# Kernel optimization log

Hardware: AMD Instinct MI355X
Metric: run time of the kernel (lower is better)

The kernel has to match this reference:

```python
import jax, jax.numpy as jnp
import numpy as np

T, N, M = 16, 10000, 2048          # timesteps, total nodes, masked nodes per step
F_IN, F1, F2, H = 256, 256, 256, 256  # feats_per_node, layer_1, layer_2, lstm_feats


def setup_inputs() -> dict:
    key = jax.random.key(0)
    ks = jax.random.split(key, 9)
    A = jax.random.normal(ks[0], (T, M, M), jnp.float32) / np.float32(np.sqrt(M))
    node_feats = jax.random.normal(ks[1], (N, F_IN), jnp.float32)
    # unique sorted indices per timestep (scatter target must be duplicate-free)
    mask = jax.vmap(lambda k: jnp.sort(jax.random.permutation(k, N)[:M]))(
        jax.random.split(ks[2], T)).astype(jnp.int32)
    u = lambda k, sh, fan: jax.random.uniform(k, sh, jnp.float32, -1.0, 1.0) * (2.0 / np.sqrt(fan))
    w0 = u(ks[3], (F_IN, F1), F_IN)
    w1 = u(ks[4], (F1, F2), F1)
    s = 1.0 / np.sqrt(H)
    W_ih = jax.random.uniform(ks[5], (4 * H, F2), jnp.float32, -s, s)
    W_hh = jax.random.uniform(ks[6], (4 * H, H), jnp.float32, -s, s)
    b_ih = jax.random.uniform(ks[7], (4 * H,), jnp.float32, -s, s)
    b_hh = jax.random.uniform(ks[8], (4 * H,), jnp.float32, -s, s)
    return {"A": A, "node_feats": node_feats, "mask": mask, "w0": w0, "w1": w1,
            "W_ih": W_ih, "W_hh": W_hh, "b_ih": b_ih, "b_hh": b_hh}


def reference(A, node_feats, mask, w0, w1, W_ih, W_hh, b_ih, b_hh):
    def gcn_step(Ah, idx):
        # layer 0: x = X @ W0 ; x[idx] = act(Ahat @ x[idx])
        x = node_feats @ w0                               # [N, F1]
        x = x.at[idx].set(jax.nn.relu(Ah @ x[idx]))
        # layer 1
        x = x @ w1                                        # [N, F2]
        x = x.at[idx].set(jax.nn.relu(Ah @ x[idx]))
        return x

    seq = jax.vmap(gcn_step)(A, mask)                     # [T, N, F2]

    def lstm_step(carry, xt):
        h, c = carry
        z = xt @ W_ih.T + h @ W_hh.T + (b_ih + b_hh)      # [N, 4H]
        i, f, g, o = jnp.split(z, 4, axis=-1)             # torch gate order i,f,g,o
        c = jax.nn.sigmoid(f) * c + jax.nn.sigmoid(i) * jnp.tanh(g)
        h = jax.nn.sigmoid(o) * jnp.tanh(c)
        return (h, c), None

    h0 = jnp.zeros((N, H), seq.dtype)
    (h, _), _ = jax.lax.scan(lstm_step, (h0, h0), seq)
    return h                                              # out[-1] of single-layer LSTM
```

## Files before the change

kernel.cpp:

```cpp
#include <hip/hip_runtime.h>
#include <cstdint>
#include <cstddef>

#pragma clang diagnostic ignored "-Waddress-space-conversion"

constexpr int T  = 16;
constexpr int N  = 10000;
constexpr int M  = 2048;
constexpr int F  = 256;
constexpr int H  = 256;
constexpr int G4 = 1024;
constexpr int NP = 10112;

typedef _Float16 f16;
using half8  = __attribute__((ext_vector_type(8))) f16;
using half4  = __attribute__((ext_vector_type(4))) f16;
using f32x4  = __attribute__((ext_vector_type(4))) float;

typedef __attribute__((address_space(1))) const void gas_t;
typedef __attribute__((address_space(3))) void las_t;

__device__ __forceinline__ void gl_lds16(const f16* g, f16* l) {
    __builtin_amdgcn_global_load_lds((gas_t*)g, (las_t*)l, 16, 0, 0);
}

__device__ __forceinline__ float fast_tanh(float x) {
    const float ax = fabsf(x);
    const float e  = __expf(-2.f * ax);
    const float t  = (1.f - e) / (1.f + e);
    return copysignf(t, x);
}

template<bool AF32, bool RELU, int OMODE>
__global__ __launch_bounds__(256, 2)
void gemm16(const void* __restrict__ Ag, long long sA,
            const f16*  __restrict__ Bg, long long sB,
            void*       __restrict__ Cg, long long sC,
            int Kk, int Nn, int Mvalid, int ldct)
{
    __shared__ f16 Als[2][128 * 32];
    __shared__ f16 Bls[2][128 * 32];

    const int tid  = threadIdx.x;
    const int lane = tid & 63;
    const int w    = tid >> 6;
    const int wm   = w >> 1, wn = w & 1;
    const int m0   = blockIdx.y * 128, n0 = blockIdx.x * 128;
    const int z    = blockIdx.z;

    const f16* Bt = Bg + (size_t)z * sB;
    const int srow = lane >> 2;
    const int scol = (lane & 3) * 8;

    f32x4 acc[4][4] = {};

    auto stage = [&](int buf, int kt) {
        const int k0 = kt * 32;
        #pragma unroll
        for (int c = 0; c < 2; ++c) {
            const int brow = w * 32 + c * 16;
            gl_lds16(Bt + (size_t)(n0 + brow + srow) * Kk + k0 + scol,
                     &Bls[buf][brow * 32]);
        }
        if constexpr (AF32) {
            const float* Af = (const float*)Ag + (size_t)z * sA;
            #pragma unroll
            for (int p = 0; p < 4; ++p) {
                const int flat = p * 1024 + tid * 4;
                const int r = flat >> 5, cc = flat & 31;
                float4 v = *(const float4*)&Af[(size_t)(m0 + r) * Kk + k0 + cc];
                half4 hv = { (f16)v.x, (f16)v.y, (f16)v.z, (f16)v.w };
                *(half4*)&Als[buf][r * 32 + cc] = hv;
            }
        } else {
            const f16* Af = (const f16*)Ag + (size_t)z * sA;
            #pragma unroll
            for (int c = 0; c < 2; ++c) {
                const int arow = w * 32 + c * 16;
                gl_lds16(Af + (size_t)(m0 + arow + srow) * Kk + k0 + scol,
                         &Als[buf][arow * 32]);
            }
        }
    };

    const int nk = Kk >> 5;
    stage(0, 0);
    int cur = 0;
    const int fr = lane & 15, fg = lane >> 4;

    for (int kt = 0; kt < nk; ++kt) {
        __syncthreads();
        if (kt + 1 < nk) stage(cur ^ 1, kt + 1);

        half8 a[4], b[4];
        #pragma unroll
        for (int i = 0; i < 4; ++i)
            a[i] = *(const half8*)&Als[cur][(wm * 64 + i * 16 + fr) * 32 + fg * 8];
        #pragma unroll
        for (int j = 0; j < 4; ++j)
            b[j] = *(const half8*)&Bls[cur][(wn * 64 + j * 16 + fr) * 32 + fg * 8];
        #pragma unroll
        for (int i = 0; i < 4; ++i)
            #pragma unroll
            for (int j = 0; j < 4; ++j)
                acc[i][j] = __builtin_amdgcn_mfma_f32_16x16x32_f16(a[i], b[j], acc[i][j], 0, 0, 0);
        cur ^= 1;
    }

    #pragma unroll
    for (int i = 0; i < 4; ++i) {
        const int gmb = m0 + wm * 64 + i * 16 + fg * 4;
        #pragma unroll
        for (int j = 0; j < 4; ++j) {
            const int gn = n0 + wn * 64 + j * 16 + fr;
            f32x4 v = acc[i][j];
            if (RELU) {
                v[0] = fmaxf(v[0], 0.f); v[1] = fmaxf(v[1], 0.f);
                v[2] = fmaxf(v[2], 0.f); v[3] = fmaxf(v[3], 0.f);
            }
            if constexpr (OMODE == 1) {
                f16* Ch = (f16*)Cg + (size_t)z * sC;
                #pragma unroll
                for (int r = 0; r < 4; ++r)
                    if (gmb + r < Mvalid) Ch[(size_t)(gmb + r) * Nn + gn] = (f16)v[r];
            } else {
                f16* Ct = (f16*)Cg + (size_t)z * sC;
                half4 hv = { (f16)v[0], (f16)v[1], (f16)v[2], (f16)v[3] };
                if (gmb + 3 < Mvalid) *(half4*)&Ct[(size_t)gn * ldct + gmb] = hv;
            }
        }
    }
}

__global__ __launch_bounds__(256, 2)
void gemm_lstm(const f16* __restrict__ h16, const f16* __restrict__ Whh,
               const f16* __restrict__ U, const f16* __restrict__ V,
               const int* __restrict__ invt, const float* __restrict__ bsum,
               float* __restrict__ Cb, f16* __restrict__ h16_out,
               float* __restrict__ hout)
{
    __shared__ f16 Als[2][128 * 32];
    __shared__ f16 Bls[2][128 * 32];

    const int tid  = threadIdx.x;
    const int lane = tid & 63;
    const int w    = tid >> 6;
    const int wm   = w >> 1, wn = w & 1;
    const int m0   = blockIdx.y * 128, n0 = blockIdx.x * 128;

    const int srow = lane >> 2;
    const int scol = (lane & 3) * 8;

    f32x4 acc[4][4] = {};

    auto stage = [&](int buf, int kt) {
        const int k0 = kt * 32;
        #pragma unroll
        for (int c = 0; c < 2; ++c) {
            const int row = w * 32 + c * 16;
            gl_lds16(Whh + (size_t)(n0 + row + srow) * H + k0 + scol, &Bls[buf][row * 32]);
            gl_lds16(h16 + (size_t)(m0 + row + srow) * H + k0 + scol, &Als[buf][row * 32]);
        }
    };

    stage(0, 0);
    int cur = 0;
    const int fr = lane & 15, fg = lane >> 4;

    for (int kt = 0; kt < H / 32; ++kt) {
        __syncthreads();
        if (kt + 1 < H / 32) stage(cur ^ 1, kt + 1);
        half8 a[4], b[4];
        #pragma unroll
        for (int i = 0; i < 4; ++i)
            a[i] = *(const half8*)&Als[cur][(wm * 64 + i * 16 + fr) * 32 + fg * 8];
        #pragma unroll
        for (int j = 0; j < 4; ++j)
            b[j] = *(const half8*)&Bls[cur][(wn * 64 + j * 16 + fr) * 32 + fg * 8];
        #pragma unroll
        for (int i = 0; i < 4; ++i)
            #pragma unroll
            for (int j = 0; j < 4; ++j)
                acc[i][j] = __builtin_amdgcn_mfma_f32_16x16x32_f16(a[i], b[j], acc[i][j], 0, 0, 0);
        cur ^= 1;
    }

    const int u = ((n0 >> 6) + wn) * 16 + fr;
    const int colbase = n0 + wn * 64 + fr;
    const float b0 = bsum[colbase], b1 = bsum[colbase + 16],
                b2 = bsum[colbase + 32], b3 = bsum[colbase + 48];
    auto sig = [](float x) { return 1.f / (1.f + __expf(-x)); };

    #pragma unroll
    for (int i = 0; i < 4; ++i) {
        const int nodeb = m0 + wm * 64 + i * 16 + fg * 4;
        #pragma unroll
        for (int r = 0; r < 4; ++r) {
            const int node = nodeb + r;
            if (node >= N) continue;
            const int p = invt[node];
            const f16* xb = (p >= 0) ? V + (size_t)p * G4 : U + (size_t)node * G4;
            const float zi = acc[i][0][r] + (float)xb[colbase]      + b0;
            const float zf = acc[i][1][r] + (float)xb[colbase + 16] + b1;
            const float zg = acc[i][2][r] + (float)xb[colbase + 32] + b2;
            const float zo = acc[i][3][r] + (float)xb[colbase + 48] + b3;
            const size_t ci = (size_t)node * H + u;
            const float c = sig(zf) * Cb[ci] + sig(zi) * fast_tanh(zg);
            Cb[ci] = c;
            const float hv = sig(zo) * fast_tanh(c);
            h16_out[ci] = (f16)hv;
            if (hout) hout[ci] = hv;
        }
    }
}

__global__ __launch_bounds__(256)
void gather_T(const f16* __restrict__ Y0h, const int* __restrict__ mask,
              f16* __restrict__ GT)
{
    __shared__ f16 tile[64][F + 8];
    const int t = blockIdx.y, p0 = blockIdx.x * 64;
    const int tid = threadIdx.x;
    const int pr = tid >> 2;
    const int fc = (tid & 3) * 8;

    const int row = mask[t * M + p0 + pr];
    const f16* src = Y0h + (size_t)row * F;
    #pragma unroll
    for (int it = 0; it < 8; ++it) {
        const int f = it * 32 + fc;
        *(half8*)&tile[pr][f] = *(const half8*)&src[f];
    }
    __syncthreads();

    f16* dst = GT + ((size_t)t * F + tid) * M + p0;
    #pragma unroll
    for (int pc = 0; pc < 64; pc += 8) {
        half8 v;
        #pragma unroll
        for (int r = 0; r < 8; ++r) v[r] = tile[pc + r][tid];
        *(half8*)&dst[pc] = v;
    }
}

__global__ void cvt_f16(const float* __restrict__ s, f16* __restrict__ d, long long n)
{
    long long base = ((long long)blockIdx.x * blockDim.x + threadIdx.x) * 4;
    if (base + 3 < n) {
        float4 v = *(const float4*)&s[base];
        half4 hv = { (f16)v.x, (f16)v.y, (f16)v.z, (f16)v.w };
        *(half4*)&d[base] = hv;
    } else {
        for (long long k = base; k < n; ++k) d[k] = (f16)s[k];
    }
}

__global__ void cvtT_f16(const float* __restrict__ s, f16* __restrict__ d, int R, int C)
{
    int i = blockIdx.x * 256 + threadIdx.x;
    if (i >= R * C) return;
    int r = i % R, c = i / R;
    d[(size_t)c * R + r] = (f16)s[(size_t)r * C + c];
}

__global__ void permW(const float* __restrict__ s, f16* __restrict__ d, int K)
{
    const int pcol = blockIdx.x;
    const int c64 = pcol >> 6, within = pcol & 63, gate = within >> 4, r = within & 15;
    const int srow = gate * 256 + c64 * 16 + r;
    const float* sp = s + (size_t)srow * K;
    f16* dp = d + (size_t)pcol * K;
    const int k = threadIdx.x * 4;
    float4 v = *(const float4*)&sp[k];
    half4 hv = { (f16)v.x, (f16)v.y, (f16)v.z, (f16)v.w };
    *(half4*)&dp[k] = hv;
}

__global__ void bias_perm(const float* __restrict__ bi, const float* __restrict__ bh,
                          float* __restrict__ bsum)
{
    const int pcol = blockIdx.x * 256 + threadIdx.x;
    if (pcol >= G4) return;
    const int c64 = pcol >> 6, within = pcol & 63, gate = within >> 4, r = within & 15;
    const int srow = gate * 256 + c64 * 16 + r;
    bsum[pcol] = bi[srow] + bh[srow];
}

__global__ void build_inv(const int* __restrict__ mask, int* __restrict__ inv)
{
    int i = blockIdx.x * blockDim.x + threadIdx.x;
    if (i >= T * M) return;
    int t = i / M;
    inv[(size_t)t * N + mask[i]] = i % M;
}

extern "C" void kernel_launch(void* const* d_in, const int* in_sizes, int n_in,
                              void* d_out, int out_size, void* d_ws, size_t ws_size,
                              hipStream_t stream)
{
    const float* A_all = (const float*)d_in[0];
    const float* nf    = (const float*)d_in[1];
    const int*   mask  = (const int*)  d_in[2];
    const float* w0    = (const float*)d_in[3];
    const float* w1    = (const float*)d_in[4];
    const float* W_ih  = (const float*)d_in[5];
    const float* W_hh  = (const float*)d_in[6];
    const float* b_ih  = (const float*)d_in[7];
    const float* b_hh  = (const float*)d_in[8];
    float* h = (float*)d_out;

    char* wp = (char*)d_ws;
    auto alloc = [&](size_t bytes) { char* p = wp; wp += (bytes + 255) & ~(size_t)255; return p; };
    f16*   nf16  = (f16*)alloc((size_t)NP * F * 2);
    f16*   w0T   = (f16*)alloc((size_t)F * F * 2);
    f16*   w1T   = (f16*)alloc((size_t)F * F * 2);
    f16*   Wih16 = (f16*)alloc((size_t)G4 * F * 2);
    f16*   Whh16 = (f16*)alloc((size_t)G4 * H * 2);
    float* bsum  = (float*)alloc((size_t)G4 * 4);
    f16*   Y0h   = (f16*)alloc((size_t)NP * F * 2);
    f16*   Y1h   = (f16*)alloc((size_t)NP * F * 2);
    f16*   Uh    = (f16*)alloc((size_t)NP * G4 * 2);
    f16*   GT    = (f16*)alloc((size_t)T * F * M * 2);
    f16*   Z1b   = (f16*)alloc((size_t)T * M * F * 2);
    f16*   Z2T   = (f16*)alloc((size_t)T * F * M * 2);
    f16*   Z3b   = (f16*)alloc((size_t)T * M * F * 2);
    f16*   Vb    = (f16*)alloc((size_t)4 * M * G4 * 2);
    float* Cb    = (float*)alloc((size_t)N * H * 4);
    f16*   h16   = (f16*)alloc((size_t)NP * H * 2);
    int*   inv   = (int*)alloc((size_t)T * N * 4);

    const size_t a16_bytes = (size_t)T * M * M * 2;
    const size_t used      = (size_t)(wp - (char*)d_ws);
    const bool   useA16    = (used + a16_bytes) <= ws_size;
    f16* A16 = useA16 ? (f16*)alloc(a16_bytes) : nullptr;

    hipMemsetAsync(Cb,  0,    (size_t)N * H * 4,  stream);
    hipMemsetAsync(h16, 0,    (size_t)NP * H * 2, stream);
    hipMemsetAsync(nf16,0,    (size_t)NP * F * 2, stream);
    hipMemsetAsync(inv, 0xFF, (size_t)T * N * 4,  stream);

    build_inv<<<(T * M + 255) / 256, 256, 0, stream>>>(mask, inv);
    cvt_f16 <<<((long long)N * F / 4 + 255) / 256, 256, 0, stream>>>(nf, nf16, (long long)N * F);
    cvtT_f16<<<(F * F + 255) / 256, 256, 0, stream>>>(w0, w0T, F, F);
    cvtT_f16<<<(F * F + 255) / 256, 256, 0, stream>>>(w1, w1T, F, F);
    permW<<<G4, 64, 0, stream>>>(W_ih, Wih16, F);
    permW<<<G4, 64, 0, stream>>>(W_hh, Whh16, H);
    bias_perm<<<(G4 + 255) / 256, 256, 0, stream>>>(b_ih, b_hh, bsum);

    gemm16<false,false,1><<<dim3(F / 128,  NP / 128, 1), 256, 0, stream>>>(nf16, 0, w0T,   0, Y0h, 0, F, F,  NP, 0);
    gemm16<false,false,1><<<dim3(F / 128,  NP / 128, 1), 256, 0, stream>>>(Y0h,  0, w1T,   0, Y1h, 0, F, F,  NP, 0);
    gemm16<false,false,1><<<dim3(G4 / 128, NP / 128, 1), 256, 0, stream>>>(Y1h,  0, Wih16, 0, Uh,  0, F, G4, NP, 0);

    gather_T<<<dim3(M / 64, T), 256, 0, stream>>>(Y0h, mask, GT);

    const long long sAmm = (long long)M * M;
    const long long sFM  = (long long)F * M;
    const long long sMF  = (long long)M * F;

    if (useA16) {
        cvt_f16<<<(int)(((long long)T * M * M / 4 + 255) / 256), 256, 0, stream>>>(
            A_all, A16, (long long)T * M * M);
        gemm16<false,true, 1><<<dim3(2, 16, T), 256, 0, stream>>>(A16, sAmm, GT,  sFM, Z1b, sMF, M, F, M, 0);
        gemm16<false,false,2><<<dim3(2, 16, T), 256, 0, stream>>>(Z1b, sMF,  w1T, 0,   Z2T, sFM, F, F, M, M);
        gemm16<false,true, 1><<<dim3(2, 16, T), 256, 0, stream>>>(A16, sAmm, Z2T, sFM, Z3b, sMF, M, F, M, 0);
    } else {
        gemm16<true, true, 1><<<dim3(2, 16, T), 256, 0, stream>>>(A_all, sAmm, GT,  sFM, Z1b, sMF, M, F, M, 0);
        gemm16<false,false,2><<<dim3(2, 16, T), 256, 0, stream>>>(Z1b,  sMF,  w1T, 0,   Z2T, sFM, F, F, M, M);
        gemm16<true, true, 1><<<dim3(2, 16, T), 256, 0, stream>>>(A_all, sAmm, Z2T, sFM, Z3b, sMF, M, F, M, 0);
    }

    for (int t = 0; t < T; ++t) {
        if ((t & 3) == 0) {
            gemm16<false,false,1><<<dim3(G4 / 128, M / 128, 4), 256, 0, stream>>>(
                Z3b + (size_t)t * M * F, sMF, Wih16, 0, Vb, (long long)M * G4, F, G4, M, 0);
        }
        gemm_lstm<<<dim3(G4 / 128, NP / 128, 1), 256, 0, stream>>>(
            h16, Whh16, Uh, Vb + (size_t)(t & 3) * M * G4, inv + (size_t)t * N,
            bsum, Cb, h16, (t == T - 1) ? h : nullptr);
    }
}
```

Before: 765.6 us.

## Fold weight chain into Uh, fuse A fp16 conversion into first GEMM, raise LSTM occupancy

Precomputes Wih·w1ᵀ·w0ᵀ as a small 1024x256 matrix so the unmasked gate inputs Uh come from one GEMM on node features, dropping the intermediate Y1h GEMM over all nodes. The standalone fp32-to-fp16 conversion pass over A is removed. Instead the first adjacency GEMM writes the converted fp16 tiles back to workspace from the n0==0 blocks, which the third GEMM then reads. gemm_lstm launch bounds go from 2 to 3 waves per SIMD, which may cause register spills. The weight reassociation changes fp16 rounding order.

```diff
diff --git a/kernel.cpp b/kernel.cpp
--- a/kernel.cpp
+++ b/kernel.cpp
@@ -31,12 +31,13 @@
     return copysignf(t, x);
 }
 
-template<bool AF32, bool RELU, int OMODE>
+template<bool AF32, bool RELU, int OMODE, bool AWB>
 __global__ __launch_bounds__(256, 2)
 void gemm16(const void* __restrict__ Ag, long long sA,
             const f16*  __restrict__ Bg, long long sB,
             void*       __restrict__ Cg, long long sC,
-            int Kk, int Nn, int Mvalid, int ldct)
+            int Kk, int Nn, int Mvalid, int ldct,
+            f16* __restrict__ a16wb)
 {
     __shared__ f16 Als[2][128 * 32];
     __shared__ f16 Bls[2][128 * 32];
@@ -71,6 +72,10 @@
                 float4 v = *(const float4*)&Af[(size_t)(m0 + r) * Kk + k0 + cc];
                 half4 hv = { (f16)v.x, (f16)v.y, (f16)v.z, (f16)v.w };
                 *(half4*)&Als[buf][r * 32 + cc] = hv;
+                if constexpr (AWB) {
+                    if (n0 == 0)
+                        *(half4*)&a16wb[(size_t)z * sA + (size_t)(m0 + r) * Kk + k0 + cc] = hv;
+                }
             }
         } else {
             const f16* Af = (const f16*)Ag + (size_t)z * sA;
@@ -132,7 +137,7 @@
     }
 }
 
-__global__ __launch_bounds__(256, 2)
+__global__ __launch_bounds__(256, 3)
 void gemm_lstm(const f16* __restrict__ h16, const f16* __restrict__ Whh,
                const f16* __restrict__ U, const f16* __restrict__ V,
                const int* __restrict__ invt, const float* __restrict__ bsum,
@@ -314,11 +319,14 @@
     f16*   nf16  = (f16*)alloc((size_t)NP * F * 2);
     f16*   w0T   = (f16*)alloc((size_t)F * F * 2);
     f16*   w1T   = (f16*)alloc((size_t)F * F * 2);
+    f16*   w0f   = (f16*)alloc((size_t)F * F * 2);
+    f16*   w1f   = (f16*)alloc((size_t)F * F * 2);
     f16*   Wih16 = (f16*)alloc((size_t)G4 * F * 2);
     f16*   Whh16 = (f16*)alloc((size_t)G4 * H * 2);
+    f16*   S1    = (f16*)alloc((size_t)G4 * F * 2);
+    f16*   S2    = (f16*)alloc((size_t)G4 * F * 2);
     float* bsum  = (float*)alloc((size_t)G4 * 4);
     f16*   Y0h   = (f16*)alloc((size_t)NP * F * 2);
-    f16*   Y1h   = (f16*)alloc((size_t)NP * F * 2);
     f16*   Uh    = (f16*)alloc((size_t)NP * G4 * 2);
     f16*   GT    = (f16*)alloc((size_t)T * F * M * 2);
     f16*   Z1b   = (f16*)alloc((size_t)T * M * F * 2);
@@ -343,13 +351,17 @@
     cvt_f16 <<<((long long)N * F / 4 + 255) / 256, 256, 0, stream>>>(nf, nf16, (long long)N * F);
     cvtT_f16<<<(F * F + 255) / 256, 256, 0, stream>>>(w0, w0T, F, F);
     cvtT_f16<<<(F * F + 255) / 256, 256, 0, stream>>>(w1, w1T, F, F);
+    cvt_f16 <<<(F * F / 4 + 255) / 256, 256, 0, stream>>>(w0, w0f, (long long)F * F);
+    cvt_f16 <<<(F * F / 4 + 255) / 256, 256, 0, stream>>>(w1, w1f, (long long)F * F);
     permW<<<G4, 64, 0, stream>>>(W_ih, Wih16, F);
     permW<<<G4, 64, 0, stream>>>(W_hh, Whh16, H);
     bias_perm<<<(G4 + 255) / 256, 256, 0, stream>>>(b_ih, b_hh, bsum);
 
-    gemm16<false,false,1><<<dim3(F / 128,  NP / 128, 1), 256, 0, stream>>>(nf16, 0, w0T,   0, Y0h, 0, F, F,  NP, 0);
-    gemm16<false,false,1><<<dim3(F / 128,  NP / 128, 1), 256, 0, stream>>>(Y0h,  0, w1T,   0, Y1h, 0, F, F,  NP, 0);
-    gemm16<false,false,1><<<dim3(G4 / 128, NP / 128, 1), 256, 0, stream>>>(Y1h,  0, Wih16, 0, Uh,  0, F, G4, NP, 0);
+    gemm16<false,false,1,false><<<dim3(2, 8, 1), 256, 0, stream>>>(Wih16, 0, w1f, 0, S1, 0, F, F, G4, 0, nullptr);
+    gemm16<false,false,1,false><<<dim3(2, 8, 1), 256, 0, stream>>>(S1,    0, w0f, 0, S2, 0, F, F, G4, 0, nullptr);
+
+    gemm16<false,false,1,false><<<dim3(F / 128,  NP / 128, 1), 256, 0, stream>>>(nf16, 0, w0T, 0, Y0h, 0, F, F,  NP, 0, nullptr);
+    gemm16<false,false,1,false><<<dim3(G4 / 128, NP / 128, 1), 256, 0, stream>>>(nf16, 0, S2,  0, Uh,  0, F, G4, NP, 0, nullptr);
 
     gather_T<<<dim3(M / 64, T), 256, 0, stream>>>(Y0h, mask, GT);
 
@@ -358,21 +370,19 @@
     const long long sMF  = (long long)M * F;
 
     if (useA16) {
-        cvt_f16<<<(int)(((long long)T * M * M / 4 + 255) / 256), 256, 0, stream>>>(
-            A_all, A16, (long long)T * M * M);
-        gemm16<false,true, 1><<<dim3(2, 16, T), 256, 0, stream>>>(A16, sAmm, GT,  sFM, Z1b, sMF, M, F, M, 0);
-        gemm16<false,false,2><<<dim3(2, 16, T), 256, 0, stream>>>(Z1b, sMF,  w1T, 0,   Z2T, sFM, F, F, M, M);
-        gemm16<false,true, 1><<<dim3(2, 16, T), 256, 0, stream>>>(A16, sAmm, Z2T, sFM, Z3b, sMF, M, F, M, 0);
+        gemm16<true, true, 1,true ><<<dim3(2, 16, T), 256, 0, stream>>>(A_all, sAmm, GT,  sFM, Z1b, sMF, M, F, M, 0, A16);
+        gemm16<false,false,2,false><<<dim3(2, 16, T), 256, 0, stream>>>(Z1b,  sMF,  w1T, 0,   Z2T, sFM, F, F, M, M, nullptr);
+        gemm16<false,true, 1,false><<<dim3(2, 16, T), 256, 0, stream>>>(A16,  sAmm, Z2T, sFM, Z3b, sMF, M, F, M, 0, nullptr);
     } else {
-        gemm16<true, true, 1><<<dim3(2, 16, T), 256, 0, stream>>>(A_all, sAmm, GT,  sFM, Z1b, sMF, M, F, M, 0);
-        gemm16<false,false,2><<<dim3(2, 16, T), 256, 0, stream>>>(Z1b,  sMF,  w1T, 0,   Z2T, sFM, F, F, M, M);
-        gemm16<true, true, 1><<<dim3(2, 16, T), 256, 0, stream>>>(A_all, sAmm, Z2T, sFM, Z3b, sMF, M, F, M, 0);
+        gemm16<true, true, 1,false><<<dim3(2, 16, T), 256, 0, stream>>>(A_all, sAmm, GT,  sFM, Z1b, sMF, M, F, M, 0, nullptr);
+        gemm16<false,false,2,false><<<dim3(2, 16, T), 256, 0, stream>>>(Z1b,  sMF,  w1T, 0,   Z2T, sFM, F, F, M, M, nullptr);
+        gemm16<true, true, 1,false><<<dim3(2, 16, T), 256, 0, stream>>>(A_all, sAmm, Z2T, sFM, Z3b, sMF, M, F, M, 0, nullptr);
     }
 
     for (int t = 0; t < T; ++t) {
         if ((t & 3) == 0) {
-            gemm16<false,false,1><<<dim3(G4 / 128, M / 128, 4), 256, 0, stream>>>(
-                Z3b + (size_t)t * M * F, sMF, Wih16, 0, Vb, (long long)M * G4, F, G4, M, 0);
+            gemm16<false,false,1,false><<<dim3(G4 / 128, M / 128, 4), 256, 0, stream>>>(
+                Z3b + (size_t)t * M * F, sMF, Wih16, 0, Vb, (long long)M * G4, F, G4, M, 0, nullptr);
         }
         gemm_lstm<<<dim3(G4 / 128, NP / 128, 1), 256, 0, stream>>>(
             h16, Whh16, Uh, Vb + (size_t)(t & 3) * M * G4, inv + (size_t)t * N,
```

Result: slower. 883.5 us (+15.4%).

## Fuse LSTM timesteps into one persistent cooperative kernel with grid sync

Applied to the files above, without the earlier changes.

Replaces the 16 per-timestep gemm_lstm launches with one cooperative kernel. It loops over timesteps, keeps the cell state in registers and ping-pongs h between two buffers, with grid.sync between steps. The V projection for all timesteps is computed up front in a single batched GEMM instead of in chunks of four. This removes launch overhead and the global read/write of C, but grid-wide sync costs something each step, and 640 blocks must be co-resident (3 per CU across 256 CUs). If that does not fit, it falls back to the per-step launches.

```diff
diff --git a/kernel.cpp b/kernel.cpp
--- a/kernel.cpp
+++ b/kernel.cpp
@@ -1,16 +1,20 @@
 #include <hip/hip_runtime.h>
+#include <hip/hip_cooperative_groups.h>
 #include <cstdint>
 #include <cstddef>
 
 #pragma clang diagnostic ignored "-Waddress-space-conversion"
 
-constexpr int T  = 16;
-constexpr int N  = 10000;
-constexpr int M  = 2048;
-constexpr int F  = 256;
-constexpr int H  = 256;
-constexpr int G4 = 1024;
-constexpr int NP = 10112;
+namespace cg = cooperative_groups;
+
+constexpr int T   = 16;
+constexpr int N   = 10000;
+constexpr int M   = 2048;
+constexpr int F   = 256;
+constexpr int H   = 256;
+constexpr int G4  = 1024;
+constexpr int NP  = 10112;
+constexpr int NP2 = 10240;
 
 typedef _Float16 f16;
 using half8  = __attribute__((ext_vector_type(8))) f16;
@@ -132,11 +136,102 @@
     }
 }
 
+__global__ __launch_bounds__(256, 3)
+void lstm_chain(const f16* __restrict__ Whh, const f16* __restrict__ U,
+                const f16* __restrict__ Vall, const int* __restrict__ invall,
+                const float* __restrict__ bsum,
+                f16* __restrict__ ha, f16* __restrict__ hb,
+                float* __restrict__ hout)
+{
+    cg::grid_group grid = cg::this_grid();
+    __shared__ f16 Als[2][128 * 32];
+    __shared__ f16 Bls[2][128 * 32];
+
+    const int tid  = threadIdx.x;
+    const int lane = tid & 63;
+    const int w    = tid >> 6;
+    const int wm   = w >> 1, wn = w & 1;
+    const int m0   = blockIdx.x * 128;
+    const int n0   = blockIdx.y * 128;
+    const int srow = lane >> 2, scol = (lane & 3) * 8;
+    const int fr   = lane & 15, fg = lane >> 4;
+
+    const int u = ((n0 >> 6) + wn) * 16 + fr;
+    const int colbase = n0 + wn * 64 + fr;
+    const float b0 = bsum[colbase],      b1 = bsum[colbase + 16],
+                b2 = bsum[colbase + 32], b3 = bsum[colbase + 48];
+    auto sig = [](float x) { return 1.f / (1.f + __expf(-x)); };
+
+    float creg[4][4] = {};
+    const f16* hin = ha;
+    f16*       hnx = hb;
+
+    for (int t = 0; t < T; ++t) {
+        const f16* V    = Vall   + (size_t)t * M * G4;
+        const int* invt = invall + (size_t)t * N;
+
+        f32x4 acc[4][4] = {};
+        auto stageh = [&](int buf, int kt) {
+            const int k0 = kt * 32;
+            #pragma unroll
+            for (int c = 0; c < 2; ++c) {
+                const int row = w * 32 + c * 16;
+                gl_lds16(Whh + (size_t)(n0 + row + srow) * H + k0 + scol, &Bls[buf][row * 32]);
+                gl_lds16(hin + (size_t)(m0 + row + srow) * H + k0 + scol, &Als[buf][row * 32]);
+            }
+        };
+        stageh(0, 0);
+        int cur = 0;
+        #pragma unroll
+        for (int kt = 0; kt < H / 32; ++kt) {
+            __syncthreads();
+            if (kt + 1 < H / 32) stageh(cur ^ 1, kt + 1);
+            half8 a[4], b[4];
+            #pragma unroll
+            for (int i = 0; i < 4; ++i)
+                a[i] = *(const half8*)&Als[cur][(wm * 64 + i * 16 + fr) * 32 + fg * 8];
+            #pragma unroll
+            for (int j = 0; j < 4; ++j)
+                b[j] = *(const half8*)&Bls[cur][(wn * 64 + j * 16 + fr) * 32 + fg * 8];
+            #pragma unroll
+            for (int i = 0; i < 4; ++i)
+                #pragma unroll
+                for (int j = 0; j < 4; ++j)
+                    acc[i][j] = __builtin_amdgcn_mfma_f32_16x16x32_f16(a[i], b[j], acc[i][j], 0, 0, 0);
+            cur ^= 1;
+        }
+
+        #pragma unroll
+        for (int i = 0; i < 4; ++i) {
+            const int nodeb = m0 + wm * 64 + i * 16 + fg * 4;
+            #pragma unroll
+            for (int r = 0; r < 4; ++r) {
+                const int node = nodeb + r;
+                if (node < N) {
+                    const int p = invt[node];
+                    const f16* xb = (p >= 0) ? V + (size_t)p * G4 : U + (size_t)node * G4;
+                    const float zi = acc[i][0][r] + (float)xb[colbase]      + b0;
+                    const float zf = acc[i][1][r] + (float)xb[colbase + 16] + b1;
+                    const float zg = acc[i][2][r] + (float)xb[colbase + 32] + b2;
+                    const float zo = acc[i][3][r] + (float)xb[colbase + 48] + b3;
+                    const float c  = sig(zf) * creg[i][r] + sig(zi) * fast_tanh(zg);
+                    creg[i][r] = c;
+                    const float hv = sig(zo) * fast_tanh(c);
+                    hnx[(size_t)node * H + u] = (f16)hv;
+                    if (t == T - 1) hout[(size_t)node * H + u] = hv;
+                }
+            }
+        }
+        grid.sync();
+        f16* tmp = (f16*)hin; hin = hnx; hnx = tmp;
+    }
+}
+
 __global__ __launch_bounds__(256, 2)
-void gemm_lstm(const f16* __restrict__ h16, const f16* __restrict__ Whh,
+void gemm_lstm(const f16* __restrict__ hin, const f16* __restrict__ Whh,
                const f16* __restrict__ U, const f16* __restrict__ V,
                const int* __restrict__ invt, const float* __restrict__ bsum,
-               float* __restrict__ Cb, f16* __restrict__ h16_out,
+               float* __restrict__ Cb, f16* __restrict__ hout16,
                float* __restrict__ hout)
 {
     __shared__ f16 Als[2][128 * 32];
@@ -147,9 +242,7 @@
     const int w    = tid >> 6;
     const int wm   = w >> 1, wn = w & 1;
     const int m0   = blockIdx.y * 128, n0 = blockIdx.x * 128;
-
-    const int srow = lane >> 2;
-    const int scol = (lane & 3) * 8;
+    const int srow = lane >> 2, scol = (lane & 3) * 8;
 
     f32x4 acc[4][4] = {};
 
@@ -159,7 +252,7 @@
         for (int c = 0; c < 2; ++c) {
             const int row = w * 32 + c * 16;
             gl_lds16(Whh + (size_t)(n0 + row + srow) * H + k0 + scol, &Bls[buf][row * 32]);
-            gl_lds16(h16 + (size_t)(m0 + row + srow) * H + k0 + scol, &Als[buf][row * 32]);
+            gl_lds16(hin + (size_t)(m0 + row + srow) * H + k0 + scol, &Als[buf][row * 32]);
         }
     };
 
@@ -187,7 +280,7 @@
 
     const int u = ((n0 >> 6) + wn) * 16 + fr;
     const int colbase = n0 + wn * 64 + fr;
-    const float b0 = bsum[colbase], b1 = bsum[colbase + 16],
+    const float b0 = bsum[colbase],      b1 = bsum[colbase + 16],
                 b2 = bsum[colbase + 32], b3 = bsum[colbase + 48];
     auto sig = [](float x) { return 1.f / (1.f + __expf(-x)); };
 
@@ -208,7 +301,7 @@
             const float c = sig(zf) * Cb[ci] + sig(zi) * fast_tanh(zg);
             Cb[ci] = c;
             const float hv = sig(zo) * fast_tanh(c);
-            h16_out[ci] = (f16)hv;
+            hout16[ci] = (f16)hv;
             if (hout) hout[ci] = hv;
         }
     }
@@ -324,9 +417,10 @@
     f16*   Z1b   = (f16*)alloc((size_t)T * M * F * 2);
     f16*   Z2T   = (f16*)alloc((size_t)T * F * M * 2);
     f16*   Z3b   = (f16*)alloc((size_t)T * M * F * 2);
-    f16*   Vb    = (f16*)alloc((size_t)4 * M * G4 * 2);
+    f16*   Vb    = (f16*)alloc((size_t)T * M * G4 * 2);
     float* Cb    = (float*)alloc((size_t)N * H * 4);
-    f16*   h16   = (f16*)alloc((size_t)NP * H * 2);
+    f16*   h16a  = (f16*)alloc((size_t)NP2 * H * 2);
+    f16*   h16b  = (f16*)alloc((size_t)NP2 * H * 2);
     int*   inv   = (int*)alloc((size_t)T * N * 4);
 
     const size_t a16_bytes = (size_t)T * M * M * 2;
@@ -334,10 +428,11 @@
     const bool   useA16    = (used + a16_bytes) <= ws_size;
     f16* A16 = useA16 ? (f16*)alloc(a16_bytes) : nullptr;
 
-    hipMemsetAsync(Cb,  0,    (size_t)N * H * 4,  stream);
-    hipMemsetAsync(h16, 0,    (size_t)NP * H * 2, stream);
-    hipMemsetAsync(nf16,0,    (size_t)NP * F * 2, stream);
-    hipMemsetAsync(inv, 0xFF, (size_t)T * N * 4,  stream);
+    hipMemsetAsync(Cb,   0,    (size_t)N * H * 4,    stream);
+    hipMemsetAsync(h16a, 0,    (size_t)NP2 * H * 2,  stream);
+    hipMemsetAsync(h16b, 0,    (size_t)NP2 * H * 2,  stream);
+    hipMemsetAsync(nf16, 0,    (size_t)NP * F * 2,   stream);
+    hipMemsetAsync(inv,  0xFF, (size_t)T * N * 4,    stream);
 
     build_inv<<<(T * M + 255) / 256, 256, 0, stream>>>(mask, inv);
     cvt_f16 <<<((long long)N * F / 4 + 255) / 256, 256, 0, stream>>>(nf, nf16, (long long)N * F);
@@ -369,13 +464,28 @@
         gemm16<true, true, 1><<<dim3(2, 16, T), 256, 0, stream>>>(A_all, sAmm, Z2T, sFM, Z3b, sMF, M, F, M, 0);
     }
 
-    for (int t = 0; t < T; ++t) {
-        if ((t & 3) == 0) {
-            gemm16<false,false,1><<<dim3(G4 / 128, M / 128, 4), 256, 0, stream>>>(
-                Z3b + (size_t)t * M * F, sMF, Wih16, 0, Vb, (long long)M * G4, F, G4, M, 0);
-        }
-        gemm_lstm<<<dim3(G4 / 128, NP / 128, 1), 256, 0, stream>>>(
-            h16, Whh16, Uh, Vb + (size_t)(t & 3) * M * G4, inv + (size_t)t * N,
-            bsum, Cb, h16, (t == T - 1) ? h : nullptr);
-    }
-}
+    gemm16<false,false,1><<<dim3(G4 / 128, M / 128, T), 256, 0, stream>>>(
+        Z3b, sMF, Wih16, 0, Vb, (long long)M * G4, F, G4, M, 0);
+
+    constexpr int NB_CHAIN = (NP2 / 128) * (G4 / 128);
+    int occ = 0;
+    bool coop = (hipOccupancyMaxActiveBlocksPerMultiprocessor(&occ, lstm_chain, 256, 0)
+                 == hipSuccess) && (occ * 256 >= NB_CHAIN);
+    if (coop) {
+        void* args[] = { (void*)&Whh16, (void*)&Uh, (void*)&Vb, (void*)&inv,
+                         (void*)&bsum, (void*)&h16a, (void*)&h16b, (void*)&h };
+        coop = hipLaunchCooperativeKernel((void*)lstm_chain, dim3(NP2 / 128, G4 / 128, 1),
+                                          dim3(256, 1, 1), args, 0, stream) == hipSuccess;
+        if (!coop) (void)hipGetLastError();
+    }
+    if (!coop) {
+        const f16* hin = h16a;
+        f16*       hnx = h16b;
+        for (int t = 0; t < T; ++t) {
+            gemm_lstm<<<dim3(G4 / 128, NP2 / 128, 1), 256, 0, stream>>>(
+                hin, Whh16, Uh, Vb + (size_t)t * M * G4, inv + (size_t)t * N,
+                bsum, Cb, hnx, (t == T - 1) ? h : nullptr);
+            f16* tmp = (f16*)hin; hin = hnx; hnx = tmp;
+        }
+    }
+}
```

After: 788.7 us. +3.0%, slower.
